# Performance work log

Hardware: AMD Instinct MI355X
Metric: run time of the kernel (lower is better)

## Reference

```python
import jax, jax.numpy as jnp
import numpy as np

L = 512       # seq_len (capped by hard-coded max_length=512)
LEN = 2048    # input feature dim ('length')
D = 2048      # d_model
H = 16        # num_heads
DH = D // H   # d_head = 128
FF = 8192     # FFN hidden
EPS = 1e-5


def _pos_encoding(n, d):
    # Matches PositionalEncoderLayer buffer construction exactly.
    pos = jnp.arange(n, dtype=jnp.float32)[:, None]                              # [n,1]
    freqs = 1.0 / (2.0 * jnp.pi) / (10000.0 * jnp.exp(jnp.arange(0, d, 2, dtype=jnp.float32) / d))
    pe = jnp.zeros((n, d), dtype=jnp.float32)
    pe = pe.at[:, 0::2].set(jnp.sin(2.0 * jnp.pi * freqs * pos))
    pe = pe.at[:, 1::2].set(jnp.cos(2.0 * jnp.pi * freqs * pos))
    return pe


def _layernorm(x, g, b):
    mu = jnp.mean(x, axis=-1, keepdims=True)
    var = jnp.mean((x - mu) ** 2, axis=-1, keepdims=True)
    return (x - mu) / jnp.sqrt(var + EPS) * g + b


def setup_inputs() -> dict:
    key = jax.random.key(0)
    ks = jax.random.split(key, 12)
    def lin(k, fin, fout):
        kw, kb = jax.random.split(k)
        W = jax.random.normal(kw, (fin, fout), jnp.float32) / np.sqrt(fin)
        b = jax.random.normal(kb, (fout,), jnp.float32) * 0.01
        return W, b
    emb_W, emb_b = lin(ks[0], LEN, D)
    Wq, bq = lin(ks[1], D, D)
    Wk, bk = lin(ks[2], D, D)
    Wv, bv = lin(ks[3], D, D)
    Wo, bo = lin(ks[4], D, D)
    W1, b1 = lin(ks[5], D, FF)
    W2, b2 = lin(ks[6], FF, D)
    return {
        "sequence": jax.random.normal(ks[7], (L, LEN), jnp.float32),
        "emb_W": emb_W, "emb_b": emb_b,
        "Wq": Wq, "bq": bq, "Wk": Wk, "bk": bk, "Wv": Wv, "bv": bv,
        "Wo": Wo, "bo": bo,
        "ln_g": jnp.ones((D,), jnp.float32), "ln_b": jnp.zeros((D,), jnp.float32),
        "W1": W1, "b1": b1, "W2": W2, "b2": b2,
    }


def reference(sequence, emb_W, emb_b, Wq, bq, Wk, bk, Wv, bv, Wo, bo, ln_g, ln_b, W1, b1, W2, b2):
    # Embedding + positional encoding
    X = sequence @ emb_W + emb_b                         # [L, D]
    X = X + _pos_encoding(X.shape[0], X.shape[1])
    # Multi-head attention (keeps the module's [L, d_head, H] layout)
    Q = (X @ Wq + bq).reshape(-1, DH, H)
    K = (X @ Wk + bk).reshape(-1, DH, H)
    V = (X @ Wv + bv).reshape(-1, DH, H)
    scores = jnp.einsum('ldh,mdh->lmh', Q, K) / jnp.sqrt(jnp.float32(D))  # [L, L, H]
    attn = jax.nn.softmax(scores, axis=1)                # softmax over keys
    A = jnp.einsum('lmh,mdh->ldh', attn, V).reshape(-1, D) @ Wo + bo
    # Residual + shared LayerNorm, FFN, residual + shared LayerNorm
    Xa = _layernorm(A + X, ln_g, ln_b)
    F = jax.nn.gelu(Xa @ W1 + b1) @ W2 + b2
    return _layernorm(F + Xa, ln_g, ln_b)
```

## Files before the change

kernel.cpp:

```cpp
#include <hip/hip_runtime.h>
#include <hip/hip_bf16.h>


typedef __bf16 bf16_t;
typedef __bf16 bf16x8 __attribute__((ext_vector_type(8)));
typedef float  f32x4  __attribute__((ext_vector_type(4)));

#define SEQL 512
#define DM   2048
#define FFH  8192
#define NH   16
#define DHD  128
#define PST  ((size_t)SEQL*DM)

__device__ __forceinline__ unsigned short bfbits(float f){
  bf16_t h = (bf16_t)f;
  return __builtin_bit_cast(unsigned short, h);
}
__device__ __forceinline__ unsigned int pack2(float a, float b){
  return (unsigned int)bfbits(a) | ((unsigned int)bfbits(b) << 16);
}

__device__ __forceinline__ void gll16(const bf16_t* g, bf16_t* l){
  __builtin_amdgcn_global_load_lds(
      (const __attribute__((address_space(1))) void*)g,
      (__attribute__((address_space(3))) void*)l, 16, 0, 0);
}

__global__ __launch_bounds__(256)
void cvt_bf16(const float* __restrict__ in, bf16_t* __restrict__ out){
  const int i = (blockIdx.x * 256 + threadIdx.x) * 4;
  const float4 v = *(const float4*)(in + i);
  ushort4 o;
  o.x = bfbits(v.x); o.y = bfbits(v.y); o.z = bfbits(v.z); o.w = bfbits(v.w);
  *(ushort4*)(out + i) = o;
}

struct TEnt { const float* src; bf16_t* dst; int inR, inC, tilesX, tileBase, perm, wperm; };
struct TArgs { TEnt e[7]; };

__global__ __launch_bounds__(256)
void prep_transpose(TArgs args){
  __shared__ bf16_t t[64*65];
  const int b = blockIdx.x;
  int i = 0;
#pragma unroll
  for (int j = 1; j < 7; ++j) if (b >= args.e[j].tileBase) i = j;
  const TEnt E = args.e[i];
  const int tloc = b - E.tileBase;
  const int tx = tloc % E.tilesX, ty = tloc / E.tilesX;
  const int C0 = tx * 64, R0 = ty * 64;
  const int tid = threadIdx.x;
#pragma unroll
  for (int it = 0; it < 4; ++it){
    const int ii = it*16 + (tid >> 4);
    const int j0 = (tid & 15) * 4;
    const int cc = C0 + ii;
    const int srow = E.perm ? (((cc & 127) << 4) + (cc >> 7)) : cc;
    const float4 v = *(const float4*)(E.src + (size_t)srow * E.inC + R0 + j0);
    t[(j0+0)*65 + ii] = (bf16_t)v.x;
    t[(j0+1)*65 + ii] = (bf16_t)v.y;
    t[(j0+2)*65 + ii] = (bf16_t)v.z;
    t[(j0+3)*65 + ii] = (bf16_t)v.w;
  }
  __syncthreads();
#pragma unroll
  for (int it = 0; it < 2; ++it){
    const int r  = it*32 + (tid >> 3);
    const int c0 = (tid & 7) * 8;
    unsigned short us[8];
#pragma unroll
    for (int u = 0; u < 8; ++u) us[u] = __builtin_bit_cast(unsigned short, t[r*65 + c0 + u]);
    uint4 o;
    o.x = (unsigned)us[0] | ((unsigned)us[1] << 16);
    o.y = (unsigned)us[2] | ((unsigned)us[3] << 16);
    o.z = (unsigned)us[4] | ((unsigned)us[5] << 16);
    o.w = (unsigned)us[6] | ((unsigned)us[7] << 16);
    const int orow = R0 + r;
    const int drow = E.wperm ? (((orow & 15) << 7) + (orow >> 4)) : orow;
    *(uint4*)(E.dst + (size_t)drow * E.inR + C0 + c0) = o;
  }
}

constexpr int E_PART = 0;
constexpr int E_QKV  = 1;
constexpr int E_FFN1 = 2;

template<int EPI>
__global__ __launch_bounds__(256, 4)
void gemm64(const bf16_t* __restrict__ A, const bf16_t* __restrict__ BT,
            const float* __restrict__ b0p, const float* __restrict__ b1p,
            const float* __restrict__ b2p,
            float* __restrict__ outF, bf16_t* __restrict__ o0,
            bf16_t* __restrict__ o1, bf16_t* __restrict__ o2,
            int N, int K, int Kc)
{
  __shared__ bf16_t sA[2][64*32];
  __shared__ bf16_t sB[2][128*32];
  const int tid  = threadIdx.x;
  const int lane = tid & 63, w = tid >> 6;
  const int wr = w >> 1, wc = w & 1;
  const int c = lane & 15, g = lane >> 4;
  const int m0 = blockIdx.y * 64, n0 = blockIdx.x * 128;
  const int k0 = blockIdx.z * Kc;

  const int sr = tid >> 2, ss = tid & 3;
  const int scol = ((ss ^ ((sr >> 1) & 3)) << 3);
  const bf16_t* Asrc  = A  + (size_t)(m0 + sr) * K + k0 + scol;
  const bf16_t* Bsrc0 = BT + (size_t)(n0 + sr) * K + k0 + scol;
  const bf16_t* Bsrc1 = BT + (size_t)(n0 + 64 + sr) * K + k0 + scol;

  int raA[2], raB[4];
#pragma unroll
  for (int m = 0; m < 2; ++m){
    const int r = wr*32 + m*16 + c;
    raA[m] = r*32 + ((g ^ ((r >> 1) & 3)) << 3);
  }
#pragma unroll
  for (int n = 0; n < 4; ++n){
    const int r = wc*64 + n*16 + c;
    raB[n] = r*32 + ((g ^ ((r >> 1) & 3)) << 3);
  }

#define STAGE(buf, kt) {                                      \
    gll16(Asrc  + (size_t)(kt)*32, &sA[buf][tid*8]);          \
    gll16(Bsrc0 + (size_t)(kt)*32, &sB[buf][tid*8]);          \
    gll16(Bsrc1 + (size_t)(kt)*32, &sB[buf][2048 + tid*8]);   }

  f32x4 acc[2][4] = {};
  const int nk = Kc >> 5;

  STAGE(0, 0);
  asm volatile("s_waitcnt vmcnt(0)" ::: "memory");
  __builtin_amdgcn_s_barrier();
  __builtin_amdgcn_sched_barrier(0);

  int buf = 0;
  for (int kt = 0; kt < nk; ++kt){
    if (kt + 1 < nk) STAGE(buf ^ 1, kt + 1);
    bf16x8 af[2], bq[4];
#pragma unroll
    for (int m = 0; m < 2; ++m) af[m] = *(const bf16x8*)&sA[buf][raA[m]];
#pragma unroll
    for (int n = 0; n < 4; ++n) bq[n] = *(const bf16x8*)&sB[buf][raB[n]];
#pragma unroll
    for (int m = 0; m < 2; ++m)
#pragma unroll
      for (int n = 0; n < 4; ++n)
        acc[m][n] = __builtin_amdgcn_mfma_f32_16x16x32_bf16(af[m], bq[n], acc[m][n], 0,0,0);
    asm volatile("s_waitcnt vmcnt(0)" ::: "memory");
    __builtin_amdgcn_s_barrier();
    __builtin_amdgcn_sched_barrier(0);
    buf ^= 1;
  }
#undef STAGE

#pragma unroll
  for (int n = 0; n < 4; ++n){
    const int col = n0 + wc*64 + n*16 + c;
#pragma unroll
    for (int m = 0; m < 2; ++m){
      const int row0 = m0 + wr*32 + m*16 + 4*g;
      const f32x4 a4 = acc[m][n];
      if constexpr (EPI == E_PART){
        float* dst = outF + (size_t)blockIdx.z * PST;
#pragma unroll
        for (int rr = 0; rr < 4; ++rr)
          dst[(size_t)(row0+rr)*N + col] = a4[rr];
      } else if constexpr (EPI == E_QKV){
        if (col < DM){
          const float bv = b0p[16*(col & 127) + (col >> 7)];
#pragma unroll
          for (int rr = 0; rr < 4; ++rr)
            o0[(size_t)(row0+rr)*DM + col] = (bf16_t)(a4[rr] + bv);
        } else if (col < 2*DM){
          const int cc = col - DM;
          const float bv = b1p[16*(cc & 127) + (cc >> 7)];
#pragma unroll
          for (int rr = 0; rr < 4; ++rr)
            o1[(size_t)(row0+rr)*DM + cc] = (bf16_t)(a4[rr] + bv);
        } else {
          const int cc = col - 2*DM;
          const float bv = b2p[cc];
          const int hh = cc & 15, dd = cc >> 4;
          unsigned short us[4];
#pragma unroll
          for (int rr = 0; rr < 4; ++rr) us[rr] = bfbits(a4[rr] + bv);
          *(ushort4*)&o2[(size_t)(hh*DHD + dd)*SEQL + row0] =
              make_ushort4(us[0], us[1], us[2], us[3]);
        }
      } else if constexpr (EPI == E_FFN1){
        const float bv = b0p[col];
#pragma unroll
        for (int rr = 0; rr < 4; ++rr){
          const float v = a4[rr] + bv;
          const float z = v * (v*v*0.044715f + 1.0f) * 1.5957691216f;
          const float gg = v / (1.0f + __expf(-z));
          o0[(size_t)(row0+rr)*FFH + col] = (bf16_t)gg;
        }
      }
    }
  }
}

__global__ __launch_bounds__(256)
void reduce_pos(const float* __restrict__ P, const float* __restrict__ bias,
                float* __restrict__ X, bf16_t* __restrict__ XB)
{
  const int row = blockIdx.x, c0 = threadIdx.x * 8;
  const size_t base = (size_t)row * DM + c0;
  float y[8];
#pragma unroll
  for (int j = 0; j < 8; ++j) y[j] = bias[c0 + j];
#pragma unroll
  for (int s = 0; s < 4; ++s){
    const float4 v0 = *(const float4*)(P + s*PST + base);
    const float4 v1 = *(const float4*)(P + s*PST + base + 4);
    y[0]+=v0.x; y[1]+=v0.y; y[2]+=v0.z; y[3]+=v0.w;
    y[4]+=v1.x; y[5]+=v1.y; y[6]+=v1.z; y[7]+=v1.w;
  }
#pragma unroll
  for (int j = 0; j < 8; ++j){
    const int col = c0 + j;
    const float fr  = 1e-4f * __expf(-(float)(col >> 1) * (1.0f/1024.0f));
    const float ang = (float)row * fr;
    y[j] += (col & 1) ? __cosf(ang) : __sinf(ang);
  }
  *(float4*)(X + base)     = make_float4(y[0], y[1], y[2], y[3]);
  *(float4*)(X + base + 4) = make_float4(y[4], y[5], y[6], y[7]);
  uint4 ob;
  ob.x = pack2(y[0], y[1]); ob.y = pack2(y[2], y[3]);
  ob.z = pack2(y[4], y[5]); ob.w = pack2(y[6], y[7]);
  *(uint4*)&XB[base] = ob;
}

template<int S, int WB>
__global__ __launch_bounds__(256)
void reduce_ln(const float* __restrict__ P, const float* __restrict__ bias,
               const float* __restrict__ resid, const float* __restrict__ gam,
               const float* __restrict__ bet, float* __restrict__ outF,
               bf16_t* __restrict__ outB)
{
  const int row = blockIdx.x, tid = threadIdx.x, c0 = tid * 8;
  const size_t base = (size_t)row * DM + c0;
  float y[8];
  {
    const float4 r0 = *(const float4*)(resid + base);
    const float4 r1 = *(const float4*)(resid + base + 4);
    y[0]=r0.x; y[1]=r0.y; y[2]=r0.z; y[3]=r0.w;
    y[4]=r1.x; y[5]=r1.y; y[6]=r1.z; y[7]=r1.w;
  }
#pragma unroll
  for (int j = 0; j < 8; ++j) y[j] += bias[c0 + j];
#pragma unroll
  for (int s = 0; s < S; ++s){
    const float4 v0 = *(const float4*)(P + s*PST + base);
    const float4 v1 = *(const float4*)(P + s*PST + base + 4);
    y[0]+=v0.x; y[1]+=v0.y; y[2]+=v0.z; y[3]+=v0.w;
    y[4]+=v1.x; y[5]+=v1.y; y[6]+=v1.z; y[7]+=v1.w;
  }
  float sm = 0.f, qs = 0.f;
#pragma unroll
  for (int j = 0; j < 8; ++j){ sm += y[j]; qs += y[j]*y[j]; }
#pragma unroll
  for (int off = 32; off >= 1; off >>= 1){
    sm += __shfl_xor(sm, off); qs += __shfl_xor(qs, off);
  }
  __shared__ float rs[4], rq[4];
  const int w = tid >> 6;
  if ((tid & 63) == 0){ rs[w] = sm; rq[w] = qs; }
  __syncthreads();
  sm = rs[0]+rs[1]+rs[2]+rs[3];
  qs = rq[0]+rq[1]+rq[2]+rq[3];
  const float mu   = sm * (1.0f/2048.0f);
  const float var  = qs * (1.0f/2048.0f) - mu*mu;
  const float rstd = rsqrtf(var + 1e-5f);
  const float4 g0 = *(const float4*)(gam + c0);
  const float4 g1 = *(const float4*)(gam + c0 + 4);
  const float4 b0 = *(const float4*)(bet + c0);
  const float4 b1 = *(const float4*)(bet + c0 + 4);
  float o[8];
  o[0] = (y[0]-mu)*rstd*g0.x + b0.x;  o[1] = (y[1]-mu)*rstd*g0.y + b0.y;
  o[2] = (y[2]-mu)*rstd*g0.z + b0.z;  o[3] = (y[3]-mu)*rstd*g0.w + b0.w;
  o[4] = (y[4]-mu)*rstd*g1.x + b1.x;  o[5] = (y[5]-mu)*rstd*g1.y + b1.y;
  o[6] = (y[6]-mu)*rstd*g1.z + b1.z;  o[7] = (y[7]-mu)*rstd*g1.w + b1.w;
  *(float4*)(outF + base)     = make_float4(o[0], o[1], o[2], o[3]);
  *(float4*)(outF + base + 4) = make_float4(o[4], o[5], o[6], o[7]);
  if constexpr (WB){
    uint4 ob;
    ob.x = pack2(o[0], o[1]); ob.y = pack2(o[2], o[3]);
    ob.z = pack2(o[4], o[5]); ob.w = pack2(o[6], o[7]);
    *(uint4*)&outB[base] = ob;
  }
}

__global__ __launch_bounds__(256)
void attn_kernel(const bf16_t* __restrict__ Qf, const bf16_t* __restrict__ Kf,
                 const bf16_t* __restrict__ Vt, bf16_t* __restrict__ Aout)
{
  __shared__ bf16_t Pl[32*512];
  __shared__ float redm[4][32];
  __shared__ float reds[4][32];
  const int tid = threadIdx.x;
  const int lane = tid & 63, w = tid >> 6;
  const int c = lane & 15, g = lane >> 4;
  const int h = blockIdx.y;
  const int rb = blockIdx.x * 32;
  const bf16_t* Qb = Qf + h*DHD;
  const bf16_t* Kb = Kf + h*DHD;
  const bf16_t* Vb = Vt + (size_t)h * (SEQL*DHD);

  bf16x8 qf[2][4];
#pragma unroll
  for (int a = 0; a < 2; ++a)
#pragma unroll
    for (int ks = 0; ks < 4; ++ks)
      qf[a][ks] = *(const bf16x8*)(Qb + (size_t)(rb + a*16 + c)*DM + ks*32 + g*8);

  f32x4 s[2][8] = {};
#pragma unroll
  for (int ks = 0; ks < 4; ++ks)
#pragma unroll
    for (int b = 0; b < 8; ++b){
      const bf16x8 kf = *(const bf16x8*)(Kb + (size_t)(w*128 + b*16 + c)*DM + ks*32 + g*8);
      s[0][b] = __builtin_amdgcn_mfma_f32_16x16x32_bf16(qf[0][ks], kf, s[0][b], 0,0,0);
      s[1][b] = __builtin_amdgcn_mfma_f32_16x16x32_bf16(qf[1][ks], kf, s[1][b], 0,0,0);
    }
#pragma unroll
  for (int a = 0; a < 2; ++a)
#pragma unroll
    for (int b = 0; b < 8; ++b)
#pragma unroll
      for (int rr = 0; rr < 4; ++rr) s[a][b][rr] *= 0.022097086912079612f;

  float mx[2][4], sm[2][4], inv[2][4];
#pragma unroll
  for (int a = 0; a < 2; ++a)
#pragma unroll
    for (int rr = 0; rr < 4; ++rr){
      float m = s[a][0][rr];
#pragma unroll
      for (int b = 1; b < 8; ++b) m = fmaxf(m, s[a][b][rr]);
#pragma unroll
      for (int off = 1; off < 16; off <<= 1) m = fmaxf(m, __shfl_xor(m, off));
      mx[a][rr] = m;
    }
  if (c == 0)
#pragma unroll
    for (int a = 0; a < 2; ++a)
#pragma unroll
      for (int rr = 0; rr < 4; ++rr) redm[w][a*16 + 4*g + rr] = mx[a][rr];
  __syncthreads();
#pragma unroll
  for (int a = 0; a < 2; ++a)
#pragma unroll
    for (int rr = 0; rr < 4; ++rr){
      const int lr = a*16 + 4*g + rr;
      mx[a][rr] = fmaxf(fmaxf(redm[0][lr], redm[1][lr]), fmaxf(redm[2][lr], redm[3][lr]));
      sm[a][rr] = 0.f;
    }
#pragma unroll
  for (int a = 0; a < 2; ++a)
#pragma unroll
    for (int b = 0; b < 8; ++b)
#pragma unroll
      for (int rr = 0; rr < 4; ++rr){
        const float p = __expf(s[a][b][rr] - mx[a][rr]);
        s[a][b][rr] = p;
        sm[a][rr] += p;
      }
#pragma unroll
  for (int a = 0; a < 2; ++a)
#pragma unroll
    for (int rr = 0; rr < 4; ++rr){
#pragma unroll
      for (int off = 1; off < 16; off <<= 1) sm[a][rr] += __shfl_xor(sm[a][rr], off);
    }
  if (c == 0)
#pragma unroll
    for (int a = 0; a < 2; ++a)
#pragma unroll
      for (int rr = 0; rr < 4; ++rr) reds[w][a*16 + 4*g + rr] = sm[a][rr];
  __syncthreads();
#pragma unroll
  for (int a = 0; a < 2; ++a)
#pragma unroll
    for (int rr = 0; rr < 4; ++rr){
      const int lr = a*16 + 4*g + rr;
      inv[a][rr] = 1.0f / (reds[0][lr] + reds[1][lr] + reds[2][lr] + reds[3][lr]);
    }

#pragma unroll
  for (int a = 0; a < 2; ++a)
#pragma unroll
    for (int b = 0; b < 8; ++b)
#pragma unroll
      for (int rr = 0; rr < 4; ++rr){
        const int lr  = a*16 + 4*g + rr;
        const int key = w*128 + b*16 + c;
        const int slot = (key >> 3) ^ (lr & 7);
        Pl[lr*512 + slot*8 + (key & 7)] = (bf16_t)(s[a][b][rr] * inv[a][rr]);
      }
  __syncthreads();

  f32x4 o[2][2] = {};
  const int dw = w * 32;
#pragma unroll
  for (int kst = 0; kst < 16; ++kst){
    bf16x8 pa2[2];
#pragma unroll
    for (int a = 0; a < 2; ++a){
      const int r = a*16 + c;
      const int slot = (kst*4 + g) ^ (r & 7);
      pa2[a] = *(const bf16x8*)&Pl[r*512 + slot*8];
    }
#pragma unroll
    for (int db = 0; db < 2; ++db){
      const bf16x8 vf = *(const bf16x8*)(Vb + (size_t)(dw + db*16 + c)*SEQL + kst*32 + g*8);
      o[0][db] = __builtin_amdgcn_mfma_f32_16x16x32_bf16(pa2[0], vf, o[0][db], 0,0,0);
      o[1][db] = __builtin_amdgcn_mfma_f32_16x16x32_bf16(pa2[1], vf, o[1][db], 0,0,0);
    }
  }
#pragma unroll
  for (int a = 0; a < 2; ++a)
#pragma unroll
    for (int db = 0; db < 2; ++db)
#pragma unroll
      for (int rr = 0; rr < 4; ++rr){
        const int row  = rb + a*16 + 4*g + rr;
        const int col2 = h*DHD + dw + db*16 + c;
        Aout[(size_t)row*DM + col2] = (bf16_t)o[a][db][rr];
      }
}

extern "C" void kernel_launch(void* const* d_in, const int* in_sizes, int n_in,
                              void* d_out, int out_size, void* d_ws, size_t ws_size,
                              hipStream_t stream)
{
  const float* seq   = (const float*)d_in[0];
  const float* emb_W = (const float*)d_in[1];
  const float* emb_b = (const float*)d_in[2];
  const float* Wq = (const float*)d_in[3];  const float* bq = (const float*)d_in[4];
  const float* Wk = (const float*)d_in[5];  const float* bk = (const float*)d_in[6];
  const float* Wv = (const float*)d_in[7];  const float* bv = (const float*)d_in[8];
  const float* Wo = (const float*)d_in[9];  const float* bo = (const float*)d_in[10];
  const float* ln_g = (const float*)d_in[11]; const float* ln_b = (const float*)d_in[12];
  const float* W1 = (const float*)d_in[13]; const float* b1 = (const float*)d_in[14];
  const float* W2 = (const float*)d_in[15]; const float* b2 = (const float*)d_in[16];

  char* ws = (char*)d_ws;
  size_t off = 0;
  auto take = [&](size_t bytes) -> void* {
    void* p = ws + off;
    off += (bytes + 255) & ~(size_t)255;
    return p;
  };
  bf16_t* embT  = (bf16_t*)take((size_t)DM*DM*2);
  bf16_t* WqkvT = (bf16_t*)take((size_t)3*DM*DM*2);
  bf16_t* WoTp  = (bf16_t*)take((size_t)DM*DM*2);
  bf16_t* W1T   = (bf16_t*)take((size_t)FFH*DM*2);
  bf16_t* W2T   = (bf16_t*)take((size_t)DM*FFH*2);
  bf16_t* seqB  = (bf16_t*)take((size_t)SEQL*DM*2);
  float*  X     = (float*) take((size_t)SEQL*DM*4);
  bf16_t* XB    = (bf16_t*)take((size_t)SEQL*DM*2);
  bf16_t* Qf    = (bf16_t*)take((size_t)SEQL*DM*2);
  bf16_t* Kf    = (bf16_t*)take((size_t)SEQL*DM*2);
  bf16_t* Vt    = (bf16_t*)take((size_t)SEQL*DM*2);
  bf16_t* Afl   = (bf16_t*)take((size_t)SEQL*DM*2);
  float*  Pp    = (float*) take((size_t)4*SEQL*DM*4);
  float*  Xa    = (float*) take((size_t)SEQL*DM*4);
  bf16_t* XaB   = (bf16_t*)take((size_t)SEQL*DM*2);
  bf16_t* Hb    = WqkvT;
  (void)ws_size; (void)in_sizes; (void)n_in; (void)out_size;

  cvt_bf16<<<dim3(SEQL*DM/1024), 256, 0, stream>>>(seq, seqB);
  TArgs ta;
  ta.e[0] = { emb_W, embT,                    DM,  DM,   32,    0, 0, 0 };
  ta.e[1] = { Wq,    WqkvT,                   DM,  DM,   32, 1024, 0, 1 };
  ta.e[2] = { Wk,    WqkvT + (size_t)DM*DM,   DM,  DM,   32, 2048, 0, 1 };
  ta.e[3] = { Wv,    WqkvT + (size_t)2*DM*DM, DM,  DM,   32, 3072, 0, 0 };
  ta.e[4] = { Wo,    WoTp,                    DM,  DM,   32, 4096, 1, 0 };
  ta.e[5] = { W1,    W1T,                     DM,  FFH,  32, 5120, 0, 0 };
  ta.e[6] = { W2,    W2T,                     FFH, DM,  128, 9216, 0, 0 };
  prep_transpose<<<dim3(13312), 256, 0, stream>>>(ta);

  gemm64<E_PART><<<dim3(16,8,4), 256, 0, stream>>>(seqB, embT, nullptr, nullptr, nullptr,
                                                   Pp, nullptr, nullptr, nullptr, DM, DM, 512);
  reduce_pos<<<SEQL, 256, 0, stream>>>(Pp, emb_b, X, XB);
  gemm64<E_QKV><<<dim3(48,8,1), 256, 0, stream>>>(XB, WqkvT, bq, bk, bv,
                                                  nullptr, Qf, Kf, Vt, 3*DM, DM, DM);
  attn_kernel<<<dim3(16,16), 256, 0, stream>>>(Qf, Kf, Vt, Afl);
  gemm64<E_PART><<<dim3(16,8,4), 256, 0, stream>>>(Afl, WoTp, nullptr, nullptr, nullptr,
                                                   Pp, nullptr, nullptr, nullptr, DM, DM, 512);
  reduce_ln<4,1><<<SEQL, 256, 0, stream>>>(Pp, bo, X, ln_g, ln_b, Xa, XaB);
  gemm64<E_FFN1><<<dim3(64,8,1), 256, 0, stream>>>(XaB, W1T, b1, nullptr, nullptr,
                                                   nullptr, Hb, nullptr, nullptr, FFH, DM, DM);
  gemm64<E_PART><<<dim3(16,8,4), 256, 0, stream>>>(Hb, W2T, nullptr, nullptr, nullptr,
                                                   Pp, nullptr, nullptr, nullptr, DM, FFH, 2048);
  reduce_ln<4,0><<<SEQL, 256, 0, stream>>>(Pp, b2, Xa, ln_g, ln_b, (float*)d_out, nullptr);
}
```

Baseline: 246.1 us.

## Read fp32 weights directly in GEMMs, drop the separate transpose pre-pass

Removes the prep_transpose kernel that converted all weights to transposed bf16 copies each call. The GEMMs now load fp32 weights straight from global memory, convert them to bf16 in registers and write them swizzled into LDS. Blocks are remapped through a 1D grid with an XCD-aware swizzle. Q/K no longer use a permuted weight layout; a small permute_qk kernel reorders them per head for attention. This avoids one full read/write pass over roughly 100 MB of weights, at the cost of twice the global bytes per weight tile and register-staged B loads instead of direct-to-LDS loads.

```diff
diff --git a/kernel.cpp b/kernel.cpp
--- a/kernel.cpp
+++ b/kernel.cpp
@@ -36,146 +36,135 @@
   *(ushort4*)(out + i) = o;
 }
 
-struct TEnt { const float* src; bf16_t* dst; int inR, inC, tilesX, tileBase, perm, wperm; };
-struct TArgs { TEnt e[7]; };
-
-__global__ __launch_bounds__(256)
-void prep_transpose(TArgs args){
-  __shared__ bf16_t t[64*65];
-  const int b = blockIdx.x;
-  int i = 0;
-#pragma unroll
-  for (int j = 1; j < 7; ++j) if (b >= args.e[j].tileBase) i = j;
-  const TEnt E = args.e[i];
-  const int tloc = b - E.tileBase;
-  const int tx = tloc % E.tilesX, ty = tloc / E.tilesX;
-  const int C0 = tx * 64, R0 = ty * 64;
-  const int tid = threadIdx.x;
-#pragma unroll
-  for (int it = 0; it < 4; ++it){
-    const int ii = it*16 + (tid >> 4);
-    const int j0 = (tid & 15) * 4;
-    const int cc = C0 + ii;
-    const int srow = E.perm ? (((cc & 127) << 4) + (cc >> 7)) : cc;
-    const float4 v = *(const float4*)(E.src + (size_t)srow * E.inC + R0 + j0);
-    t[(j0+0)*65 + ii] = (bf16_t)v.x;
-    t[(j0+1)*65 + ii] = (bf16_t)v.y;
-    t[(j0+2)*65 + ii] = (bf16_t)v.z;
-    t[(j0+3)*65 + ii] = (bf16_t)v.w;
-  }
-  __syncthreads();
-#pragma unroll
-  for (int it = 0; it < 2; ++it){
-    const int r  = it*32 + (tid >> 3);
-    const int c0 = (tid & 7) * 8;
-    unsigned short us[8];
-#pragma unroll
-    for (int u = 0; u < 8; ++u) us[u] = __builtin_bit_cast(unsigned short, t[r*65 + c0 + u]);
-    uint4 o;
-    o.x = (unsigned)us[0] | ((unsigned)us[1] << 16);
-    o.y = (unsigned)us[2] | ((unsigned)us[3] << 16);
-    o.z = (unsigned)us[4] | ((unsigned)us[5] << 16);
-    o.w = (unsigned)us[6] | ((unsigned)us[7] << 16);
-    const int orow = R0 + r;
-    const int drow = E.wperm ? (((orow & 15) << 7) + (orow >> 4)) : orow;
-    *(uint4*)(E.dst + (size_t)drow * E.inR + C0 + c0) = o;
-  }
-}
-
 constexpr int E_PART = 0;
 constexpr int E_QKV  = 1;
 constexpr int E_FFN1 = 2;
 
-template<int EPI>
+template<int EPI, int PERM>
 __global__ __launch_bounds__(256, 4)
-void gemm64(const bf16_t* __restrict__ A, const bf16_t* __restrict__ BT,
-            const float* __restrict__ b0p, const float* __restrict__ b1p,
-            const float* __restrict__ b2p,
-            float* __restrict__ outF, bf16_t* __restrict__ o0,
-            bf16_t* __restrict__ o1, bf16_t* __restrict__ o2,
-            int N, int K, int Kc)
+void gemmF(const bf16_t* __restrict__ A,
+           const float* __restrict__ W0p, const float* __restrict__ W1p,
+           const float* __restrict__ W2p,
+           const float* __restrict__ b0p, const float* __restrict__ b1p,
+           const float* __restrict__ b2p,
+           float* __restrict__ outF, bf16_t* __restrict__ o0,
+           bf16_t* __restrict__ o1, bf16_t* __restrict__ o2,
+           int nn, int Nw, int K, int Kc)
 {
   __shared__ bf16_t sA[2][64*32];
   __shared__ bf16_t sB[2][128*32];
   const int tid  = threadIdx.x;
   const int lane = tid & 63, w = tid >> 6;
-  const int wr = w >> 1, wc = w & 1;
+  const int wr4 = w >> 1, wc = w & 1;
   const int c = lane & 15, g = lane >> 4;
-  const int m0 = blockIdx.y * 64, n0 = blockIdx.x * 128;
-  const int k0 = blockIdx.z * Kc;
+
+  const int nwg = gridDim.x, cpx = nwg >> 3;
+  const int sblk = (blockIdx.x & 7) * cpx + (blockIdx.x >> 3);
+  const int mt = sblk & 7, q = sblk >> 3;
+  const int nt = q % nn, zt = q / nn;
+  const int m0 = mt * 64, k0 = zt * Kc;
+
+  const float* Wp = W0p; int nb0 = nt * 128;
+  if constexpr (EPI == E_QKV){
+    if (nt >= 32){ Wp = W2p; nb0 = (nt - 32) * 128; }
+    else if (nt >= 16){ Wp = W1p; nb0 = (nt - 16) * 128; }
+  }
 
   const int sr = tid >> 2, ss = tid & 3;
   const int scol = ((ss ^ ((sr >> 1) & 3)) << 3);
-  const bf16_t* Asrc  = A  + (size_t)(m0 + sr) * K + k0 + scol;
-  const bf16_t* Bsrc0 = BT + (size_t)(n0 + sr) * K + k0 + scol;
-  const bf16_t* Bsrc1 = BT + (size_t)(n0 + 64 + sr) * K + k0 + scol;
+  const bf16_t* Asrc = A + (size_t)(m0 + sr) * K + k0 + scol;
+
+  const int bn4 = tid & 31;
+  const int kb  = (tid >> 5) * 4;
+  const float* Bsrc = Wp + nb0 + bn4 * 4;
 
   int raA[2], raB[4];
 #pragma unroll
   for (int m = 0; m < 2; ++m){
-    const int r = wr*32 + m*16 + c;
+    const int r = wr4*32 + m*16 + c;
     raA[m] = r*32 + ((g ^ ((r >> 1) & 3)) << 3);
   }
 #pragma unroll
   for (int n = 0; n < 4; ++n){
     const int r = wc*64 + n*16 + c;
-    raB[n] = r*32 + ((g ^ ((r >> 1) & 3)) << 3);
-  }
-
-#define STAGE(buf, kt) {                                      \
-    gll16(Asrc  + (size_t)(kt)*32, &sA[buf][tid*8]);          \
-    gll16(Bsrc0 + (size_t)(kt)*32, &sB[buf][tid*8]);          \
-    gll16(Bsrc1 + (size_t)(kt)*32, &sB[buf][2048 + tid*8]);   }
+    raB[n] = r*32 + ((g ^ ((r >> 2) & 3)) << 3);
+  }
+
+  f32x4 wr[4];
+
+#define LOADW(kt) {                                                         \
+    const int kk = k0 + (kt)*32 + kb;                                       \
+    _Pragma("unroll")                                                       \
+    for (int i = 0; i < 4; ++i){                                            \
+      const int kr = kk + i;                                                \
+      const int krow = PERM ? (((kr & 127) << 4) + (kr >> 7)) : kr;         \
+      wr[i] = *(const f32x4*)(Bsrc + (size_t)krow * Nw);                    \
+    } }
+
+#define STAGEA(bf, kt) gll16(Asrc + (size_t)(kt)*32, &sA[bf][tid*8]);
+
+#define WRITEB(bf) {                                                        \
+    _Pragma("unroll")                                                       \
+    for (int j = 0; j < 4; ++j){                                            \
+      const int n = bn4*4 + j;                                              \
+      const int el = n*32 + (kb ^ (((n >> 2) & 3) << 3));                   \
+      uint2 v2;                                                             \
+      v2.x = pack2(wr[0][j], wr[1][j]);                                     \
+      v2.y = pack2(wr[2][j], wr[3][j]);                                     \
+      *(uint2*)&sB[bf][el] = v2;                                            \
+    } }
 
   f32x4 acc[2][4] = {};
   const int nk = Kc >> 5;
 
-  STAGE(0, 0);
-  asm volatile("s_waitcnt vmcnt(0)" ::: "memory");
-  __builtin_amdgcn_s_barrier();
-  __builtin_amdgcn_sched_barrier(0);
+  LOADW(0);
+  STAGEA(0, 0);
+  WRITEB(0);
+  __syncthreads();
 
   int buf = 0;
   for (int kt = 0; kt < nk; ++kt){
-    if (kt + 1 < nk) STAGE(buf ^ 1, kt + 1);
-    bf16x8 af[2], bq[4];
+    const int nb = buf ^ 1;
+    if (kt + 1 < nk){ LOADW(kt + 1); STAGEA(nb, kt + 1); }
+    bf16x8 af[2], bq4[4];
 #pragma unroll
     for (int m = 0; m < 2; ++m) af[m] = *(const bf16x8*)&sA[buf][raA[m]];
 #pragma unroll
-    for (int n = 0; n < 4; ++n) bq[n] = *(const bf16x8*)&sB[buf][raB[n]];
+    for (int n = 0; n < 4; ++n) bq4[n] = *(const bf16x8*)&sB[buf][raB[n]];
 #pragma unroll
     for (int m = 0; m < 2; ++m)
 #pragma unroll
       for (int n = 0; n < 4; ++n)
-        acc[m][n] = __builtin_amdgcn_mfma_f32_16x16x32_bf16(af[m], bq[n], acc[m][n], 0,0,0);
-    asm volatile("s_waitcnt vmcnt(0)" ::: "memory");
-    __builtin_amdgcn_s_barrier();
-    __builtin_amdgcn_sched_barrier(0);
-    buf ^= 1;
-  }
-#undef STAGE
+        acc[m][n] = __builtin_amdgcn_mfma_f32_16x16x32_bf16(af[m], bq4[n], acc[m][n], 0,0,0);
+    if (kt + 1 < nk){ WRITEB(nb); }
+    __syncthreads();
+    buf = nb;
+  }
+#undef LOADW
+#undef STAGEA
+#undef WRITEB
 
 #pragma unroll
   for (int n = 0; n < 4; ++n){
-    const int col = n0 + wc*64 + n*16 + c;
+    const int col = nt*128 + wc*64 + n*16 + c;
 #pragma unroll
     for (int m = 0; m < 2; ++m){
-      const int row0 = m0 + wr*32 + m*16 + 4*g;
+      const int row0 = m0 + wr4*32 + m*16 + 4*g;
       const f32x4 a4 = acc[m][n];
       if constexpr (EPI == E_PART){
-        float* dst = outF + (size_t)blockIdx.z * PST;
+        float* dst = outF + (size_t)zt * PST;
 #pragma unroll
         for (int rr = 0; rr < 4; ++rr)
-          dst[(size_t)(row0+rr)*N + col] = a4[rr];
+          dst[(size_t)(row0+rr)*DM + col] = a4[rr];
       } else if constexpr (EPI == E_QKV){
         if (col < DM){
-          const float bv = b0p[16*(col & 127) + (col >> 7)];
+          const float bv = b0p[col];
 #pragma unroll
           for (int rr = 0; rr < 4; ++rr)
             o0[(size_t)(row0+rr)*DM + col] = (bf16_t)(a4[rr] + bv);
         } else if (col < 2*DM){
           const int cc = col - DM;
-          const float bv = b1p[16*(cc & 127) + (cc >> 7)];
+          const float bv = b1p[cc];
 #pragma unroll
           for (int rr = 0; rr < 4; ++rr)
             o1[(size_t)(row0+rr)*DM + cc] = (bf16_t)(a4[rr] + bv);
@@ -204,6 +193,165 @@
 }
 
 __global__ __launch_bounds__(256)
+void permute_qk(const bf16_t* __restrict__ Qf, const bf16_t* __restrict__ Kf,
+                bf16_t* __restrict__ Qhd, bf16_t* __restrict__ Khd)
+{
+  const int row = blockIdx.x, which = blockIdx.y, tid = threadIdx.x;
+  const bf16_t* src = (which ? Kf : Qf) + (size_t)row * DM;
+  bf16_t* dst = which ? Khd : Qhd;
+  const int hh = tid >> 4, d0 = (tid & 15) * 8;
+  unsigned short us[8];
+#pragma unroll
+  for (int j = 0; j < 8; ++j)
+    us[j] = __builtin_bit_cast(unsigned short, src[(d0 + j)*NH + hh]);
+  uint4 o;
+  o.x = (unsigned)us[0] | ((unsigned)us[1] << 16);
+  o.y = (unsigned)us[2] | ((unsigned)us[3] << 16);
+  o.z = (unsigned)us[4] | ((unsigned)us[5] << 16);
+  o.w = (unsigned)us[6] | ((unsigned)us[7] << 16);
+  *(uint4*)&dst[(size_t)hh*(SEQL*DHD) + (size_t)row*DHD + d0] = o;
+}
+
+__global__ __launch_bounds__(256)
+void attn_kernel(const bf16_t* __restrict__ Qh, const bf16_t* __restrict__ Kh,
+                 const bf16_t* __restrict__ Vt, bf16_t* __restrict__ Aout)
+{
+  __shared__ bf16_t Pl[32*512];
+  __shared__ float redm[4][32];
+  __shared__ float reds[4][32];
+  const int tid = threadIdx.x;
+  const int lane = tid & 63, w = tid >> 6;
+  const int c = lane & 15, g = lane >> 4;
+  const int h = blockIdx.y;
+  const int rb = blockIdx.x * 32;
+  const bf16_t* Qb = Qh + (size_t)h * (SEQL*DHD);
+  const bf16_t* Kb = Kh + (size_t)h * (SEQL*DHD);
+  const bf16_t* Vb = Vt + (size_t)h * (SEQL*DHD);
+
+  bf16x8 qf[2][4];
+#pragma unroll
+  for (int a = 0; a < 2; ++a)
+#pragma unroll
+    for (int ks = 0; ks < 4; ++ks)
+      qf[a][ks] = *(const bf16x8*)(Qb + (size_t)(rb + a*16 + c)*DHD + ks*32 + g*8);
+
+  f32x4 s[2][8] = {};
+#pragma unroll
+  for (int ks = 0; ks < 4; ++ks)
+#pragma unroll
+    for (int b = 0; b < 8; ++b){
+      const bf16x8 kf = *(const bf16x8*)(Kb + (size_t)(w*128 + b*16 + c)*DHD + ks*32 + g*8);
+      s[0][b] = __builtin_amdgcn_mfma_f32_16x16x32_bf16(qf[0][ks], kf, s[0][b], 0,0,0);
+      s[1][b] = __builtin_amdgcn_mfma_f32_16x16x32_bf16(qf[1][ks], kf, s[1][b], 0,0,0);
+    }
+#pragma unroll
+  for (int a = 0; a < 2; ++a)
+#pragma unroll
+    for (int b = 0; b < 8; ++b)
+#pragma unroll
+      for (int rr = 0; rr < 4; ++rr) s[a][b][rr] *= 0.022097086912079612f;
+
+  float mx[2][4], sm[2][4], inv[2][4];
+#pragma unroll
+  for (int a = 0; a < 2; ++a)
+#pragma unroll
+    for (int rr = 0; rr < 4; ++rr){
+      float m = s[a][0][rr];
+#pragma unroll
+      for (int b = 1; b < 8; ++b) m = fmaxf(m, s[a][b][rr]);
+#pragma unroll
+      for (int off = 1; off < 16; off <<= 1) m = fmaxf(m, __shfl_xor(m, off));
+      mx[a][rr] = m;
+    }
+  if (c == 0)
+#pragma unroll
+    for (int a = 0; a < 2; ++a)
+#pragma unroll
+      for (int rr = 0; rr < 4; ++rr) redm[w][a*16 + 4*g + rr] = mx[a][rr];
+  __syncthreads();
+#pragma unroll
+  for (int a = 0; a < 2; ++a)
+#pragma unroll
+    for (int rr = 0; rr < 4; ++rr){
+      const int lr = a*16 + 4*g + rr;
+      mx[a][rr] = fmaxf(fmaxf(redm[0][lr], redm[1][lr]), fmaxf(redm[2][lr], redm[3][lr]));
+      sm[a][rr] = 0.f;
+    }
+#pragma unroll
+  for (int a = 0; a < 2; ++a)
+#pragma unroll
+    for (int b = 0; b < 8; ++b)
+#pragma unroll
+      for (int rr = 0; rr < 4; ++rr){
+        const float p = __expf(s[a][b][rr] - mx[a][rr]);
+        s[a][b][rr] = p;
+        sm[a][rr] += p;
+      }
+#pragma unroll
+  for (int a = 0; a < 2; ++a)
+#pragma unroll
+    for (int rr = 0; rr < 4; ++rr){
+#pragma unroll
+      for (int off = 1; off < 16; off <<= 1) sm[a][rr] += __shfl_xor(sm[a][rr], off);
+    }
+  if (c == 0)
+#pragma unroll
+    for (int a = 0; a < 2; ++a)
+#pragma unroll
+      for (int rr = 0; rr < 4; ++rr) reds[w][a*16 + 4*g + rr] = sm[a][rr];
+  __syncthreads();
+#pragma unroll
+  for (int a = 0; a < 2; ++a)
+#pragma unroll
+    for (int rr = 0; rr < 4; ++rr){
+      const int lr = a*16 + 4*g + rr;
+      inv[a][rr] = 1.0f / (reds[0][lr] + reds[1][lr] + reds[2][lr] + reds[3][lr]);
+    }
+
+#pragma unroll
+  for (int a = 0; a < 2; ++a)
+#pragma unroll
+    for (int b = 0; b < 8; ++b)
+#pragma unroll
+      for (int rr = 0; rr < 4; ++rr){
+        const int lr  = a*16 + 4*g + rr;
+        const int key = w*128 + b*16 + c;
+        const int slot = (key >> 3) ^ (lr & 7);
+        Pl[lr*512 + slot*8 + (key & 7)] = (bf16_t)(s[a][b][rr] * inv[a][rr]);
+      }
+  __syncthreads();
+
+  f32x4 o[2][2] = {};
+  const int dw = w * 32;
+#pragma unroll
+  for (int kst = 0; kst < 16; ++kst){
+    bf16x8 pa2[2];
+#pragma unroll
+    for (int a = 0; a < 2; ++a){
+      const int r = a*16 + c;
+      const int slot = (kst*4 + g) ^ (r & 7);
+      pa2[a] = *(const bf16x8*)&Pl[r*512 + slot*8];
+    }
+#pragma unroll
+    for (int db = 0; db < 2; ++db){
+      const bf16x8 vf = *(const bf16x8*)(Vb + (size_t)(dw + db*16 + c)*SEQL + kst*32 + g*8);
+      o[0][db] = __builtin_amdgcn_mfma_f32_16x16x32_bf16(pa2[0], vf, o[0][db], 0,0,0);
+      o[1][db] = __builtin_amdgcn_mfma_f32_16x16x32_bf16(pa2[1], vf, o[1][db], 0,0,0);
+    }
+  }
+#pragma unroll
+  for (int a = 0; a < 2; ++a)
+#pragma unroll
+    for (int db = 0; db < 2; ++db)
+#pragma unroll
+      for (int rr = 0; rr < 4; ++rr){
+        const int row  = rb + a*16 + 4*g + rr;
+        const int col2 = h*DHD + dw + db*16 + c;
+        Aout[(size_t)row*DM + col2] = (bf16_t)o[a][db][rr];
+      }
+}
+
+__global__ __launch_bounds__(256)
 void reduce_pos(const float* __restrict__ P, const float* __restrict__ bias,
                 float* __restrict__ X, bf16_t* __restrict__ XB)
 {
@@ -234,7 +382,7 @@
   *(uint4*)&XB[base] = ob;
 }
 
-template<int S, int WB>
+template<int WB>
 __global__ __launch_bounds__(256)
 void reduce_ln(const float* __restrict__ P, const float* __restrict__ bias,
                const float* __restrict__ resid, const float* __restrict__ gam,
@@ -253,7 +401,7 @@
 #pragma unroll
   for (int j = 0; j < 8; ++j) y[j] += bias[c0 + j];
 #pragma unroll
-  for (int s = 0; s < S; ++s){
+  for (int s = 0; s < 4; ++s){
     const float4 v0 = *(const float4*)(P + s*PST + base);
     const float4 v1 = *(const float4*)(P + s*PST + base + 4);
     y[0]+=v0.x; y[1]+=v0.y; y[2]+=v0.z; y[3]+=v0.w;
@@ -294,145 +442,6 @@
   }
 }
 
-__global__ __launch_bounds__(256)
-void attn_kernel(const bf16_t* __restrict__ Qf, const bf16_t* __restrict__ Kf,
-                 const bf16_t* __restrict__ Vt, bf16_t* __restrict__ Aout)
-{
-  __shared__ bf16_t Pl[32*512];
-  __shared__ float redm[4][32];
-  __shared__ float reds[4][32];
-  const int tid = threadIdx.x;
-  const int lane = tid & 63, w = tid >> 6;
-  const int c = lane & 15, g = lane >> 4;
-  const int h = blockIdx.y;
-  const int rb = blockIdx.x * 32;
-  const bf16_t* Qb = Qf + h*DHD;
-  const bf16_t* Kb = Kf + h*DHD;
-  const bf16_t* Vb = Vt + (size_t)h * (SEQL*DHD);
-
-  bf16x8 qf[2][4];
-#pragma unroll
-  for (int a = 0; a < 2; ++a)
-#pragma unroll
-    for (int ks = 0; ks < 4; ++ks)
-      qf[a][ks] = *(const bf16x8*)(Qb + (size_t)(rb + a*16 + c)*DM + ks*32 + g*8);
-
-  f32x4 s[2][8] = {};
-#pragma unroll
-  for (int ks = 0; ks < 4; ++ks)
-#pragma unroll
-    for (int b = 0; b < 8; ++b){
-      const bf16x8 kf = *(const bf16x8*)(Kb + (size_t)(w*128 + b*16 + c)*DM + ks*32 + g*8);
-      s[0][b] = __builtin_amdgcn_mfma_f32_16x16x32_bf16(qf[0][ks], kf, s[0][b], 0,0,0);
-      s[1][b] = __builtin_amdgcn_mfma_f32_16x16x32_bf16(qf[1][ks], kf, s[1][b], 0,0,0);
-    }
-#pragma unroll
-  for (int a = 0; a < 2; ++a)
-#pragma unroll
-    for (int b = 0; b < 8; ++b)
-#pragma unroll
-      for (int rr = 0; rr < 4; ++rr) s[a][b][rr] *= 0.022097086912079612f;
-
-  float mx[2][4], sm[2][4], inv[2][4];
-#pragma unroll
-  for (int a = 0; a < 2; ++a)
-#pragma unroll
-    for (int rr = 0; rr < 4; ++rr){
-      float m = s[a][0][rr];
-#pragma unroll
-      for (int b = 1; b < 8; ++b) m = fmaxf(m, s[a][b][rr]);
-#pragma unroll
-      for (int off = 1; off < 16; off <<= 1) m = fmaxf(m, __shfl_xor(m, off));
-      mx[a][rr] = m;
-    }
-  if (c == 0)
-#pragma unroll
-    for (int a = 0; a < 2; ++a)
-#pragma unroll
-      for (int rr = 0; rr < 4; ++rr) redm[w][a*16 + 4*g + rr] = mx[a][rr];
-  __syncthreads();
-#pragma unroll
-  for (int a = 0; a < 2; ++a)
-#pragma unroll
-    for (int rr = 0; rr < 4; ++rr){
-      const int lr = a*16 + 4*g + rr;
-      mx[a][rr] = fmaxf(fmaxf(redm[0][lr], redm[1][lr]), fmaxf(redm[2][lr], redm[3][lr]));
-      sm[a][rr] = 0.f;
-    }
-#pragma unroll
-  for (int a = 0; a < 2; ++a)
-#pragma unroll
-    for (int b = 0; b < 8; ++b)
-#pragma unroll
-      for (int rr = 0; rr < 4; ++rr){
-        const float p = __expf(s[a][b][rr] - mx[a][rr]);
-        s[a][b][rr] = p;
-        sm[a][rr] += p;
-      }
-#pragma unroll
-  for (int a = 0; a < 2; ++a)
-#pragma unroll
-    for (int rr = 0; rr < 4; ++rr){
-#pragma unroll
-      for (int off = 1; off < 16; off <<= 1) sm[a][rr] += __shfl_xor(sm[a][rr], off);
-    }
-  if (c == 0)
-#pragma unroll
-    for (int a = 0; a < 2; ++a)
-#pragma unroll
-      for (int rr = 0; rr < 4; ++rr) reds[w][a*16 + 4*g + rr] = sm[a][rr];
-  __syncthreads();
-#pragma unroll
-  for (int a = 0; a < 2; ++a)
-#pragma unroll
-    for (int rr = 0; rr < 4; ++rr){
-      const int lr = a*16 + 4*g + rr;
-      inv[a][rr] = 1.0f / (reds[0][lr] + reds[1][lr] + reds[2][lr] + reds[3][lr]);
-    }
-
-#pragma unroll
-  for (int a = 0; a < 2; ++a)
-#pragma unroll
-    for (int b = 0; b < 8; ++b)
-#pragma unroll
-      for (int rr = 0; rr < 4; ++rr){
-        const int lr  = a*16 + 4*g + rr;
-        const int key = w*128 + b*16 + c;
-        const int slot = (key >> 3) ^ (lr & 7);
-        Pl[lr*512 + slot*8 + (key & 7)] = (bf16_t)(s[a][b][rr] * inv[a][rr]);
-      }
-  __syncthreads();
-
-  f32x4 o[2][2] = {};
-  const int dw = w * 32;
-#pragma unroll
-  for (int kst = 0; kst < 16; ++kst){
-    bf16x8 pa2[2];
-#pragma unroll
-    for (int a = 0; a < 2; ++a){
-      const int r = a*16 + c;
-      const int slot = (kst*4 + g) ^ (r & 7);
-      pa2[a] = *(const bf16x8*)&Pl[r*512 + slot*8];
-    }
-#pragma unroll
-    for (int db = 0; db < 2; ++db){
-      const bf16x8 vf = *(const bf16x8*)(Vb + (size_t)(dw + db*16 + c)*SEQL + kst*32 + g*8);
-      o[0][db] = __builtin_amdgcn_mfma_f32_16x16x32_bf16(pa2[0], vf, o[0][db], 0,0,0);
-      o[1][db] = __builtin_amdgcn_mfma_f32_16x16x32_bf16(pa2[1], vf, o[1][db], 0,0,0);
-    }
-  }
-#pragma unroll
-  for (int a = 0; a < 2; ++a)
-#pragma unroll
-    for (int db = 0; db < 2; ++db)
-#pragma unroll
-      for (int rr = 0; rr < 4; ++rr){
-        const int row  = rb + a*16 + 4*g + rr;
-        const int col2 = h*DHD + dw + db*16 + c;
-        Aout[(size_t)row*DM + col2] = (bf16_t)o[a][db][rr];
-      }
-}
-
 extern "C" void kernel_launch(void* const* d_in, const int* in_sizes, int n_in,
                               void* d_out, int out_size, void* d_ws, size_t ws_size,
                               hipStream_t stream)
@@ -455,47 +464,41 @@
     off += (bytes + 255) & ~(size_t)255;
     return p;
   };
-  bf16_t* embT  = (bf16_t*)take((size_t)DM*DM*2);
-  bf16_t* WqkvT = (bf16_t*)take((size_t)3*DM*DM*2);
-  bf16_t* WoTp  = (bf16_t*)take((size_t)DM*DM*2);
-  bf16_t* W1T   = (bf16_t*)take((size_t)FFH*DM*2);
-  bf16_t* W2T   = (bf16_t*)take((size_t)DM*FFH*2);
-  bf16_t* seqB  = (bf16_t*)take((size_t)SEQL*DM*2);
-  float*  X     = (float*) take((size_t)SEQL*DM*4);
-  bf16_t* XB    = (bf16_t*)take((size_t)SEQL*DM*2);
-  bf16_t* Qf    = (bf16_t*)take((size_t)SEQL*DM*2);
-  bf16_t* Kf    = (bf16_t*)take((size_t)SEQL*DM*2);
-  bf16_t* Vt    = (bf16_t*)take((size_t)SEQL*DM*2);
-  bf16_t* Afl   = (bf16_t*)take((size_t)SEQL*DM*2);
-  float*  Pp    = (float*) take((size_t)4*SEQL*DM*4);
-  float*  Xa    = (float*) take((size_t)SEQL*DM*4);
-  bf16_t* XaB   = (bf16_t*)take((size_t)SEQL*DM*2);
-  bf16_t* Hb    = WqkvT;
+  bf16_t* seqB = (bf16_t*)take((size_t)SEQL*DM*2);
+  float*  X    = (float*) take((size_t)SEQL*DM*4);
+  bf16_t* XB   = (bf16_t*)take((size_t)SEQL*DM*2);
+  bf16_t* Qf   = (bf16_t*)take((size_t)SEQL*DM*2);
+  bf16_t* Kf   = (bf16_t*)take((size_t)SEQL*DM*2);
+  bf16_t* Qhd  = (bf16_t*)take((size_t)SEQL*DM*2);
+  bf16_t* Khd  = (bf16_t*)take((size_t)SEQL*DM*2);
+  bf16_t* Vt   = (bf16_t*)take((size_t)SEQL*DM*2);
+  bf16_t* Afl  = (bf16_t*)take((size_t)SEQL*DM*2);
+  float*  Pp   = (float*) take((size_t)4*SEQL*DM*4);
+  float*  Xa   = (float*) take((size_t)SEQL*DM*4);
+  bf16_t* XaB  = (bf16_t*)take((size_t)SEQL*DM*2);
+  bf16_t* Hb   = (bf16_t*)take((size_t)SEQL*FFH*2);
   (void)ws_size; (void)in_sizes; (void)n_in; (void)out_size;
 
   cvt_bf16<<<dim3(SEQL*DM/1024), 256, 0, stream>>>(seq, seqB);
-  TArgs ta;
-  ta.e[0] = { emb_W, embT,                    DM,  DM,   32,    0, 0, 0 };
-  ta.e[1] = { Wq,    WqkvT,                   DM,  DM,   32, 1024, 0, 1 };
-  ta.e[2] = { Wk,    WqkvT + (size_t)DM*DM,   DM,  DM,   32, 2048, 0, 1 };
-  ta.e[3] = { Wv,    WqkvT + (size_t)2*DM*DM, DM,  DM,   32, 3072, 0, 0 };
-  ta.e[4] = { Wo,    WoTp,                    DM,  DM,   32, 4096, 1, 0 };
-  ta.e[5] = { W1,    W1T,                     DM,  FFH,  32, 5120, 0, 0 };
-  ta.e[6] = { W2,    W2T,                     FFH, DM,  128, 9216, 0, 0 };
-  prep_transpose<<<dim3(13312), 256, 0, stream>>>(ta);
-
-  gemm64<E_PART><<<dim3(16,8,4), 256, 0, stream>>>(seqB, embT, nullptr, nullptr, nullptr,
-                                                   Pp, nullptr, nullptr, nullptr, DM, DM, 512);
+
+  gemmF<E_PART,0><<<dim3(512), 256, 0, stream>>>(seqB, emb_W, nullptr, nullptr,
+      nullptr, nullptr, nullptr, Pp, nullptr, nullptr, nullptr, 16, DM, DM, 512);
   reduce_pos<<<SEQL, 256, 0, stream>>>(Pp, emb_b, X, XB);
-  gemm64<E_QKV><<<dim3(48,8,1), 256, 0, stream>>>(XB, WqkvT, bq, bk, bv,
-                                                  nullptr, Qf, Kf, Vt, 3*DM, DM, DM);
-  attn_kernel<<<dim3(16,16), 256, 0, stream>>>(Qf, Kf, Vt, Afl);
-  gemm64<E_PART><<<dim3(16,8,4), 256, 0, stream>>>(Afl, WoTp, nullptr, nullptr, nullptr,
-                                                   Pp, nullptr, nullptr, nullptr, DM, DM, 512);
-  reduce_ln<4,1><<<SEQL, 256, 0, stream>>>(Pp, bo, X, ln_g, ln_b, Xa, XaB);
-  gemm64<E_FFN1><<<dim3(64,8,1), 256, 0, stream>>>(XaB, W1T, b1, nullptr, nullptr,
-                                                   nullptr, Hb, nullptr, nullptr, FFH, DM, DM);
-  gemm64<E_PART><<<dim3(16,8,4), 256, 0, stream>>>(Hb, W2T, nullptr, nullptr, nullptr,
-                                                   Pp, nullptr, nullptr, nullptr, DM, FFH, 2048);
-  reduce_ln<4,0><<<SEQL, 256, 0, stream>>>(Pp, b2, Xa, ln_g, ln_b, (float*)d_out, nullptr);
-}
+
+  gemmF<E_QKV,0><<<dim3(384), 256, 0, stream>>>(XB, Wq, Wk, Wv,
+      bq, bk, bv, nullptr, Qf, Kf, Vt, 48, DM, DM, DM);
+  permute_qk<<<dim3(SEQL,2), 256, 0, stream>>>(Qf, Kf, Qhd, Khd);
+
+  attn_kernel<<<dim3(16,16), 256, 0, stream>>>(Qhd, Khd, Vt, Afl);
+
+  gemmF<E_PART,1><<<dim3(512), 256, 0, stream>>>(Afl, Wo, nullptr, nullptr,
+      nullptr, nullptr, nullptr, Pp, nullptr, nullptr, nullptr, 16, DM, DM, 512);
+  reduce_ln<1><<<SEQL, 256, 0, stream>>>(Pp, bo, X, ln_g, ln_b, Xa, XaB);
+
+  gemmF<E_FFN1,0><<<dim3(512), 256, 0, stream>>>(XaB, W1, nullptr, nullptr,
+      b1, nullptr, nullptr, nullptr, Hb, nullptr, nullptr, 64, FFH, DM, DM);
+
+  gemmF<E_PART,0><<<dim3(512), 256, 0, stream>>>(Hb, W2, nullptr, nullptr,
+      nullptr, nullptr, nullptr, Pp, nullptr, nullptr, nullptr, 16, DM, FFH, 2048);
+  reduce_ln<0><<<SEQL, 256, 0, stream>>>(Pp, b2, Xa, ln_g, ln_b, (float*)d_out, nullptr);
+}
```

New measurement: 262.2 us. 1.07x slower.
